# Performance work log

Hardware: AMD Instinct MI355X
Metric: run time of the kernel (lower is better)

## Reference

```python
import jax, jax.numpy as jnp
import numpy as np

N_NODES = 100000
N_EDGES = 3200000


def gcn_conv(x, src, dst, ew, W, b, num_nodes):
    """PyG GCNConv: h = x@W; out[dst] += norm * h[src]; norm = d^-1/2[src]*w*d^-1/2[dst].
    src/dst/ew must already include self-loops (weight 1)."""
    h = x @ W  # [N, F_out]
    deg = jax.ops.segment_sum(ew, dst, num_segments=num_nodes)  # weighted in-degree
    dinv = jnp.where(deg > 0, jax.lax.rsqrt(deg), 0.0)
    norm = dinv[src] * ew * dinv[dst]  # [E]
    msg = h[src] * norm[:, None]  # [E, F_out] gather + scale
    out = jax.ops.segment_sum(msg, dst, num_segments=num_nodes)  # scatter-add
    return out + b


def setup_inputs() -> dict:
    key = jax.random.key(0)
    k1, k2, k3, k4, k5 = jax.random.split(key, 5)
    x = jax.random.normal(k1, (N_NODES, 35), dtype=jnp.float32)
    edge_index = jax.random.randint(k2, (2, N_EDGES), 0, N_NODES, dtype=jnp.int64)
    edge_weight = jax.random.uniform(k3, (N_EDGES,), dtype=jnp.float32)
    W1 = jax.random.normal(k4, (35, 64), dtype=jnp.float32) * (1.0 / np.sqrt(35))
    b1 = jnp.zeros((64,), dtype=jnp.float32)
    W2 = jax.random.normal(k5, (64, 2), dtype=jnp.float32) * (1.0 / np.sqrt(64))
    b2 = jnp.zeros((2,), dtype=jnp.float32)
    return {"x": x, "edge_index": edge_index, "edge_weight": edge_weight,
            "W1": W1, "b1": b1, "W2": W2, "b2": b2}


def reference(x, edge_index, edge_weight, W1, b1, W2, b2):
    n = x.shape[0]
    # add self-loops with weight 1 (PyG default fill_value=1), static shapes
    loop = jnp.arange(n, dtype=edge_index.dtype)
    src = jnp.concatenate([edge_index[0], loop])
    dst = jnp.concatenate([edge_index[1], loop])
    ew = jnp.concatenate([edge_weight, jnp.ones((n,), dtype=edge_weight.dtype)])

    h = jax.nn.relu(gcn_conv(x, src, dst, ew, W1, b1, n))
    h = gcn_conv(h, src, dst, ew, W2, b2, n)
    return jax.nn.log_softmax(h, axis=1)
```

## Files before the change

### kernel.cpp

```cpp
#include <hip/hip_runtime.h>
#include <hip/hip_fp16.h>
#include <math.h>

#define FIN 35
#define F1  64
#define BSZ 256
#define BSH 8
#define GSH 7
#define MAXNB 512
#define PCH 8192
#define SCAP 12288

__global__ void k_hist(const int* __restrict__ dst, int* __restrict__ cmat,
                       int E, int NB, int NCHUNK) {
    __shared__ int h[MAXNB];
    int c = blockIdx.x, t = threadIdx.x;
    for (int i = t; i < NB; i += 256) h[i] = 0;
    __syncthreads();
    int e0 = c * PCH, e1 = min(e0 + PCH, E);
    bool al = ((size_t)(dst + e0) & 15) == 0;
    int nv = al ? ((e1 - e0) >> 2) : 0;
    const int4* d4 = (const int4*)(dst + e0);
    for (int i = t; i < nv; i += 256) {
        int4 v = d4[i];
        atomicAdd(&h[v.x >> BSH], 1); atomicAdd(&h[v.y >> BSH], 1);
        atomicAdd(&h[v.z >> BSH], 1); atomicAdd(&h[v.w >> BSH], 1);
    }
    for (int e = e0 + (nv << 2) + t; e < e1; e += 256) atomicAdd(&h[dst[e] >> BSH], 1);
    __syncthreads();
    for (int i = t; i < NB; i += 256) cmat[(size_t)i * NCHUNK + c] = h[i];
}

__global__ void k_scan_row(int* __restrict__ cmat, int* __restrict__ rsum, int NCHUNK) {
    __shared__ int s[512];
    int b = blockIdx.x, t = threadIdx.x;
    int v = (t < NCHUNK) ? cmat[(size_t)b * NCHUNK + t] : 0;
    s[t] = v;
    __syncthreads();
    #pragma unroll
    for (int off = 1; off < 512; off <<= 1) {
        int tv = (t >= off) ? s[t - off] : 0;
        __syncthreads();
        s[t] += tv;
        __syncthreads();
    }
    if (t < NCHUNK) cmat[(size_t)b * NCHUNK + t] = s[t] - v;
    if (t == 511) rsum[b] = s[511];
}

__global__ void k_scan_buck(const int* __restrict__ rsum, int* __restrict__ bbase,
                            int* __restrict__ boff, int NB, int E) {
    __shared__ int s[1024];
    int t = threadIdx.x;
    int v = (t < NB) ? rsum[t] : 0;
    s[t] = v;
    __syncthreads();
    #pragma unroll
    for (int off = 1; off < 1024; off <<= 1) {
        int tv = (t >= off) ? s[t - off] : 0;
        __syncthreads();
        s[t] += tv;
        __syncthreads();
    }
    if (t < NB) {
        int excl = s[t] - v;
        bbase[t] = excl;
        boff[t] = excl;
    }
    if (t == 0) boff[NB] = E;
}

__global__ __launch_bounds__(512) void k_place(
        const int* __restrict__ src, const int* __restrict__ dst,
        const float* __restrict__ ew, const int* __restrict__ cmat,
        const int* __restrict__ bbase,
        int2* __restrict__ recs, int E, int NB, int NCHUNK) {
    extern __shared__ char pmem[];
    int2* lrec = (int2*)pmem;
    __shared__ int s[512];
    __shared__ int lbase[512];
    __shared__ int cur[512];
    __shared__ int gwin[512];
    int c = blockIdx.x, t = threadIdx.x;
    s[t] = 0;
    __syncthreads();
    int e0 = c * PCH, e1 = min(e0 + PCH, E);
    bool al = (((size_t)(dst + e0) | (size_t)(src + e0) | (size_t)(ew + e0)) & 15) == 0;
    int nv = al ? ((e1 - e0) >> 2) : 0;
    const int4*   s4 = (const int4*)(src + e0);
    const int4*   d4 = (const int4*)(dst + e0);
    const float4* w4 = (const float4*)(ew + e0);
    for (int i = t; i < nv; i += 512) {
        int4 v = d4[i];
        atomicAdd(&s[v.x >> BSH], 1); atomicAdd(&s[v.y >> BSH], 1);
        atomicAdd(&s[v.z >> BSH], 1); atomicAdd(&s[v.w >> BSH], 1);
    }
    for (int e = e0 + (nv << 2) + t; e < e1; e += 512) atomicAdd(&s[dst[e] >> BSH], 1);
    __syncthreads();
    int v = s[t];
    __syncthreads();
    #pragma unroll
    for (int off = 1; off < 512; off <<= 1) {
        int tv = (t >= off) ? s[t - off] : 0;
        __syncthreads();
        s[t] += tv;
        __syncthreads();
    }
    lbase[t] = s[t] - v;
    cur[t] = 0;
    gwin[t] = (t < NB) ? (cmat[(size_t)t * NCHUNK + c] + bbase[t]) : 0;
    __syncthreads();
    for (int i = t; i < nv; i += 512) {
        int4   sv = s4[i];
        int4   dv = d4[i];
        float4 wv = w4[i];
        int b, r;
        b = dv.x >> BSH; r = atomicAdd(&cur[b], 1);
        lrec[lbase[b] + r] = make_int2(sv.x | ((dv.x & (BSZ-1)) << 24), __float_as_int(wv.x));
        b = dv.y >> BSH; r = atomicAdd(&cur[b], 1);
        lrec[lbase[b] + r] = make_int2(sv.y | ((dv.y & (BSZ-1)) << 24), __float_as_int(wv.y));
        b = dv.z >> BSH; r = atomicAdd(&cur[b], 1);
        lrec[lbase[b] + r] = make_int2(sv.z | ((dv.z & (BSZ-1)) << 24), __float_as_int(wv.z));
        b = dv.w >> BSH; r = atomicAdd(&cur[b], 1);
        lrec[lbase[b] + r] = make_int2(sv.w | ((dv.w & (BSZ-1)) << 24), __float_as_int(wv.w));
    }
    for (int e = e0 + (nv << 2) + t; e < e1; e += 512) {
        int d = dst[e];
        int b = d >> BSH;
        int r = atomicAdd(&cur[b], 1);
        lrec[lbase[b] + r] = make_int2(src[e] | ((d & (BSZ-1)) << 24), __float_as_int(ew[e]));
    }
    __syncthreads();
    int hw = t >> 5, sl = t & 31;
    for (int b = hw; b < NB; b += 16) {
        int lb = lbase[b], cn = cur[b], gw = gwin[b];
        for (int i = sl; i < cn; i += 32) recs[gw + i] = lrec[lb + i];
    }
}

__global__ __launch_bounds__(512) void k_sort(
        const int* __restrict__ boff, const int2* __restrict__ recs_in,
        int2* __restrict__ recs_out, int* __restrict__ row_ptr,
        float* __restrict__ dinv, const float* __restrict__ x,
        const float* __restrict__ W1, __half* __restrict__ g1, int n) {
    extern __shared__ char smem[];
    unsigned short* inv16 = (unsigned short*)smem;
    float* xs  = (float*)smem;
    float* W1s = (float*)(smem + (size_t)BSZ * FIN * 4);
    __shared__ int   hcnt[BSZ];
    __shared__ int   hoff[BSZ];
    __shared__ float dsum[BSZ];
    int b = blockIdx.x, t = threadIdx.x;
    if (t < BSZ) { hcnt[t] = 0; dsum[t] = 1.0f; }
    __syncthreads();
    int s0 = boff[b], s1 = boff[b + 1];
    int cnt = s1 - s0;
    for (int i = t; i < cnt; i += 512) {
        int2 rc = recs_in[s0 + i];
        int dl = ((unsigned)rc.x) >> 24;
        atomicAdd(&hcnt[dl], 1);
        atomicAdd(&dsum[dl], __int_as_float(rc.y));
    }
    __syncthreads();
    int v = 0;
    if (t < BSZ) { v = hcnt[t]; hoff[t] = v; }
    __syncthreads();
    #pragma unroll
    for (int off = 1; off < BSZ; off <<= 1) {
        int tv = 0;
        if (t < BSZ && t >= off) tv = hoff[t - off];
        __syncthreads();
        if (t < BSZ) hoff[t] += tv;
        __syncthreads();
    }
    if (t < BSZ) {
        int excl = hoff[t] - v;
        int node = b * BSZ + t;
        if (node < n) {
            row_ptr[node] = s0 + excl;
            dinv[node] = rsqrtf(dsum[t]);
            if (node == n - 1) row_ptr[n] = s1;
        }
        hcnt[t] = excl;
    }
    __syncthreads();
    if (cnt <= SCAP) {
        for (int i = t; i < cnt; i += 512) {
            int2 rc = recs_in[s0 + i];
            int dl = ((unsigned)rc.x) >> 24;
            int pos = atomicAdd(&hcnt[dl], 1);
            inv16[pos] = (unsigned short)i;
        }
        __syncthreads();
        for (int o = t; o < cnt; o += 512) {
            int2 rc = recs_in[s0 + inv16[o]];
            recs_out[s0 + o] = make_int2((rc.x & 0xFFFFFF) << GSH, rc.y);
        }
    } else {
        for (int i = t; i < cnt; i += 512) {
            int2 rc = recs_in[s0 + i];
            int dl = ((unsigned)rc.x) >> 24;
            int pos = atomicAdd(&hcnt[dl], 1);
            recs_out[s0 + pos] = make_int2((rc.x & 0xFFFFFF) << GSH, rc.y);
        }
    }
    __syncthreads();
    int row0 = b * BSZ;
    int nrows = min(BSZ, n - row0);
    if (nrows <= 0) return;
    for (int i = t; i < (FIN * F1) / 4; i += 512) ((float4*)W1s)[i] = ((const float4*)W1)[i];
    const float* xbase = x + (size_t)row0 * FIN;
    int tot = nrows * FIN;
    int totv = tot >> 2;
    for (int i = t; i < totv; i += 512) ((float4*)xs)[i] = ((const float4*)xbase)[i];
    for (int i = (totv << 2) + t; i < tot; i += 512) xs[i] = xbase[i];
    __syncthreads();
    int f = t & 63, w8 = t >> 6;
    for (int nl = w8; nl < nrows; nl += 8) {
        float acc = 0.0f;
        #pragma unroll
        for (int k = 0; k < FIN; k++) acc += xs[nl * FIN + k] * W1s[k * F1 + f];
        g1[(size_t)(row0 + nl) * F1 + f] = __float2half(acc * rsqrtf(dsum[nl]));
    }
}

__global__ void k_gather1(const int* __restrict__ rp, const int2* __restrict__ csr,
                          const __half* __restrict__ g1,
                          const float* __restrict__ dinv, const float* __restrict__ b1,
                          const float* __restrict__ W2, float* __restrict__ g2, int n) {
    int wid = (int)((blockIdx.x * (long long)blockDim.x + threadIdx.x) >> 6);
    int f = threadIdx.x & 63;
    if (wid >= n) return;
    const char* g1b = (const char*)g1 + f * 2;
    int start = rp[wid], end = rp[wid + 1];
    float acc = 0.0f;
    int e = start;
    for (; e + 16 <= end; e += 16) {
        float a[16];
        int2 r[16];
        #pragma unroll
        for (int j = 0; j < 16; j++) r[j] = csr[e + j];
        #pragma unroll
        for (int j = 0; j < 16; j++)
            a[j] = __half2float(*(const __half*)(g1b + (unsigned)r[j].x));
        #pragma unroll
        for (int j = 0; j < 16; j++) acc += __int_as_float(r[j].y) * a[j];
    }
    for (; e + 4 <= end; e += 4) {
        int2 r0 = csr[e], r1 = csr[e+1], r2 = csr[e+2], r3 = csr[e+3];
        float a0 = __half2float(*(const __half*)(g1b + (unsigned)r0.x));
        float a1 = __half2float(*(const __half*)(g1b + (unsigned)r1.x));
        float a2 = __half2float(*(const __half*)(g1b + (unsigned)r2.x));
        float a3 = __half2float(*(const __half*)(g1b + (unsigned)r3.x));
        acc += __int_as_float(r0.y) * a0; acc += __int_as_float(r1.y) * a1;
        acc += __int_as_float(r2.y) * a2; acc += __int_as_float(r3.y) * a3;
    }
    for (; e < end; e++) {
        int2 r = csr[e];
        acc += __int_as_float(r.y) * __half2float(*(const __half*)(g1b + (unsigned)r.x));
    }
    float dv = dinv[wid];
    float h = dv * (acc + __half2float(g1[(size_t)wid * F1 + f])) + b1[f];
    h = h > 0.0f ? h : 0.0f;
    float2 w2v = ((const float2*)W2)[f];
    float z0 = h * w2v.x, z1 = h * w2v.y;
    #pragma unroll
    for (int off = 32; off > 0; off >>= 1) {
        z0 += __shfl_xor(z0, off, 64);
        z1 += __shfl_xor(z1, off, 64);
    }
    if (f == 0) {
        g2[(size_t)wid * 2 + 0] = dv * z0;
        g2[(size_t)wid * 2 + 1] = dv * z1;
    }
}

__global__ void k_gather2(const int* __restrict__ rp, const int2* __restrict__ csr,
                          const float* __restrict__ g2,
                          const float* __restrict__ dinv, const float* __restrict__ b2,
                          float* __restrict__ out, int n) {
    int w = (int)((blockIdx.x * (long long)blockDim.x + threadIdx.x) >> 6);
    int lane = threadIdx.x & 63;
    int half = lane >> 5, sub = lane & 31;
    int node = w * 2 + half;
    if (node >= n) return;
    const char* g2b = (const char*)g2;
    int start = rp[node], end = rp[node + 1];
    float a0 = 0.0f, a1 = 0.0f;
    int e = start + sub;
    for (; e + 96 < end; e += 128) {
        int2 q0 = csr[e], q1 = csr[e + 32], q2 = csr[e + 64], q3 = csr[e + 96];
        float2 v0 = *(const float2*)(g2b + (((unsigned)q0.x) >> 4));
        float2 v1 = *(const float2*)(g2b + (((unsigned)q1.x) >> 4));
        float2 v2 = *(const float2*)(g2b + (((unsigned)q2.x) >> 4));
        float2 v3 = *(const float2*)(g2b + (((unsigned)q3.x) >> 4));
        a0 += __int_as_float(q0.y) * v0.x; a1 += __int_as_float(q0.y) * v0.y;
        a0 += __int_as_float(q1.y) * v1.x; a1 += __int_as_float(q1.y) * v1.y;
        a0 += __int_as_float(q2.y) * v2.x; a1 += __int_as_float(q2.y) * v2.y;
        a0 += __int_as_float(q3.y) * v3.x; a1 += __int_as_float(q3.y) * v3.y;
    }
    for (; e < end; e += 32) {
        int2 r = csr[e];
        float wt = __int_as_float(r.y);
        float2 gv = *(const float2*)(g2b + (((unsigned)r.x) >> 4));
        a0 += wt * gv.x; a1 += wt * gv.y;
    }
    #pragma unroll
    for (int off = 16; off > 0; off >>= 1) {
        a0 += __shfl_xor(a0, off, 64);
        a1 += __shfl_xor(a1, off, 64);
    }
    if (sub == 0) {
        float dv = dinv[node];
        float2 sv = ((const float2*)g2)[node];
        float z0 = dv * (a0 + sv.x) + b2[0];
        float z1 = dv * (a1 + sv.y) + b2[1];
        float m = fmaxf(z0, z1);
        float lse = m + logf(expf(z0 - m) + expf(z1 - m));
        ((float2*)out)[node] = make_float2(z0 - lse, z1 - lse);
    }
}

extern "C" void kernel_launch(void* const* d_in, const int* in_sizes, int n_in,
                              void* d_out, int out_size, void* d_ws, size_t ws_size,
                              hipStream_t stream) {
    const float* x  = (const float*)d_in[0];
    const int*   ei = (const int*)d_in[1];
    const float* ew = (const float*)d_in[2];
    const float* W1 = (const float*)d_in[3];
    const float* b1 = (const float*)d_in[4];
    const float* W2 = (const float*)d_in[5];
    const float* b2 = (const float*)d_in[6];
    float* out = (float*)d_out;

    int n = in_sizes[0] / FIN;
    int E = in_sizes[2];
    const int* src = ei;
    const int* dst = ei + E;
    int NB = (n + BSZ - 1) / BSZ;
    int NCHUNK = (E + PCH - 1) / PCH;
    int M = NB * NCHUNK;

    char* ws = (char*)d_ws;
    size_t off = 0;
    auto alloc = [&](size_t bytes) -> void* {
        void* p = ws + off;
        off += (bytes + 15) & ~(size_t)15;
        return p;
    };
    int*    cmat    = (int*)   alloc((size_t)M * 4);
    int*    rsum    = (int*)   alloc((size_t)NB * 4);
    int*    bbase   = (int*)   alloc((size_t)NB * 4);
    int*    boff    = (int*)   alloc((size_t)(NB + 1) * 4);
    int*    row_ptr = (int*)   alloc((size_t)(n + 1) * 4);
    float*  dinv    = (float*) alloc((size_t)n * 4);
    int2*   recs_a  = (int2*)  alloc((size_t)E * 8);
    int2*   recs_b  = (int2*)  alloc((size_t)E * 8);
    __half* g1      = (__half*)alloc((size_t)n * F1 * 2);
    float*  g2      = (float*) alloc((size_t)n * 2 * 4);

    size_t place_lds = (size_t)PCH * 8;
    size_t sort_lds  = (size_t)BSZ * FIN * 4 + (size_t)FIN * F1 * 4;

    int g2_waves = (n + 1) / 2 + 1;

    k_hist     <<<NCHUNK, 256, 0, stream>>>(dst, cmat, E, NB, NCHUNK);
    k_scan_row <<<NB, 512, 0, stream>>>(cmat, rsum, NCHUNK);
    k_scan_buck<<<1, 1024, 0, stream>>>(rsum, bbase, boff, NB, E);
    k_place    <<<NCHUNK, 512, place_lds, stream>>>(src, dst, ew, cmat, bbase, recs_a, E, NB, NCHUNK);
    k_sort     <<<NB, 512, sort_lds, stream>>>(boff, recs_a, recs_b, row_ptr, dinv, x, W1, g1, n);
    k_gather1  <<<(n + 3) / 4, 256, 0, stream>>>(row_ptr, recs_b, g1, dinv, b1, W2, g2, n);
    k_gather2  <<<(g2_waves + 3) / 4, 256, 0, stream>>>(row_ptr, recs_b, g2, dinv, b2, out, n);
}
```

Baseline: 291.7 us.

## Replace per-chunk count matrix scan with global atomic bucket counters

Drops the chunk-by-bucket count matrix and its per-row scan kernel. The histogram kernel now atomically accumulates global bucket totals, and the placement kernel claims its write window in each bucket with an atomicAdd on a per-bucket cursor. This removes one kernel launch and the matrix traffic, at the cost of a memset and contended global atomics. Edge order within a bucket also becomes nondeterministic, which the later per-bucket sort should absorb.

New measurement: 324.0 us. 1.11x slower.

```diff
diff --git a/kernel.cpp b/kernel.cpp
--- a/kernel.cpp
+++ b/kernel.cpp
@@ -11,8 +11,8 @@
 #define PCH 8192
 #define SCAP 12288
 
-__global__ void k_hist(const int* __restrict__ dst, int* __restrict__ cmat,
-                       int E, int NB, int NCHUNK) {
+__global__ void k_hist(const int* __restrict__ dst, int* __restrict__ kcnt,
+                       int E, int NB) {
     __shared__ int h[MAXNB];
     int c = blockIdx.x, t = threadIdx.x;
     for (int i = t; i < NB; i += 256) h[i] = 0;
@@ -28,31 +28,14 @@
     }
     for (int e = e0 + (nv << 2) + t; e < e1; e += 256) atomicAdd(&h[dst[e] >> BSH], 1);
     __syncthreads();
-    for (int i = t; i < NB; i += 256) cmat[(size_t)i * NCHUNK + c] = h[i];
-}
-
-__global__ void k_scan_row(int* __restrict__ cmat, int* __restrict__ rsum, int NCHUNK) {
-    __shared__ int s[512];
-    int b = blockIdx.x, t = threadIdx.x;
-    int v = (t < NCHUNK) ? cmat[(size_t)b * NCHUNK + t] : 0;
-    s[t] = v;
-    __syncthreads();
-    #pragma unroll
-    for (int off = 1; off < 512; off <<= 1) {
-        int tv = (t >= off) ? s[t - off] : 0;
-        __syncthreads();
-        s[t] += tv;
-        __syncthreads();
-    }
-    if (t < NCHUNK) cmat[(size_t)b * NCHUNK + t] = s[t] - v;
-    if (t == 511) rsum[b] = s[511];
-}
-
-__global__ void k_scan_buck(const int* __restrict__ rsum, int* __restrict__ bbase,
+    for (int i = t; i < NB; i += 256) { int v = h[i]; if (v) atomicAdd(&kcnt[i], v); }
+}
+
+__global__ void k_scan_buck(const int* __restrict__ kcnt, int* __restrict__ bbase,
                             int* __restrict__ boff, int NB, int E) {
     __shared__ int s[1024];
     int t = threadIdx.x;
-    int v = (t < NB) ? rsum[t] : 0;
+    int v = (t < NB) ? kcnt[t] : 0;
     s[t] = v;
     __syncthreads();
     #pragma unroll
@@ -72,9 +55,9 @@
 
 __global__ __launch_bounds__(512) void k_place(
         const int* __restrict__ src, const int* __restrict__ dst,
-        const float* __restrict__ ew, const int* __restrict__ cmat,
-        const int* __restrict__ bbase,
-        int2* __restrict__ recs, int E, int NB, int NCHUNK) {
+        const float* __restrict__ ew, const int* __restrict__ bbase,
+        int* __restrict__ gcur,
+        int2* __restrict__ recs, int E, int NB) {
     extern __shared__ char pmem[];
     int2* lrec = (int2*)pmem;
     __shared__ int s[512];
@@ -108,7 +91,7 @@
     }
     lbase[t] = s[t] - v;
     cur[t] = 0;
-    gwin[t] = (t < NB) ? (cmat[(size_t)t * NCHUNK + c] + bbase[t]) : 0;
+    gwin[t] = (t < NB && v > 0) ? (bbase[t] + atomicAdd(&gcur[t], v)) : 0;
     __syncthreads();
     for (int i = t; i < nv; i += 512) {
         int4   sv = s4[i];
@@ -339,7 +322,6 @@
     const int* dst = ei + E;
     int NB = (n + BSZ - 1) / BSZ;
     int NCHUNK = (E + PCH - 1) / PCH;
-    int M = NB * NCHUNK;
 
     char* ws = (char*)d_ws;
     size_t off = 0;
@@ -348,8 +330,9 @@
         off += (bytes + 15) & ~(size_t)15;
         return p;
     };
-    int*    cmat    = (int*)   alloc((size_t)M * 4);
-    int*    rsum    = (int*)   alloc((size_t)NB * 4);
+    int*    cnts    = (int*)   alloc((size_t)2 * NB * 4);
+    int*    kcnt    = cnts;
+    int*    gcur    = cnts + NB;
     int*    bbase   = (int*)   alloc((size_t)NB * 4);
     int*    boff    = (int*)   alloc((size_t)(NB + 1) * 4);
     int*    row_ptr = (int*)   alloc((size_t)(n + 1) * 4);
@@ -364,10 +347,10 @@
 
     int g2_waves = (n + 1) / 2 + 1;
 
-    k_hist     <<<NCHUNK, 256, 0, stream>>>(dst, cmat, E, NB, NCHUNK);
-    k_scan_row <<<NB, 512, 0, stream>>>(cmat, rsum, NCHUNK);
-    k_scan_buck<<<1, 1024, 0, stream>>>(rsum, bbase, boff, NB, E);
-    k_place    <<<NCHUNK, 512, place_lds, stream>>>(src, dst, ew, cmat, bbase, recs_a, E, NB, NCHUNK);
+    hipMemsetAsync(cnts, 0, (size_t)2 * NB * 4, stream);
+    k_hist     <<<NCHUNK, 256, 0, stream>>>(dst, kcnt, E, NB);
+    k_scan_buck<<<1, 1024, 0, stream>>>(kcnt, bbase, boff, NB, E);
+    k_place    <<<NCHUNK, 512, place_lds, stream>>>(src, dst, ew, bbase, gcur, recs_a, E, NB);
     k_sort     <<<NB, 512, sort_lds, stream>>>(boff, recs_a, recs_b, row_ptr, dinv, x, W1, g1, n);
     k_gather1  <<<(n + 3) / 4, 256, 0, stream>>>(row_ptr, recs_b, g1, dinv, b1, W2, g2, n);
     k_gather2  <<<(g2_waves + 3) / 4, 256, 0, stream>>>(row_ptr, recs_b, g2, dinv, b2, out, n);
```
